# Kernel optimization log

Measured on AMD Instinct MI355X. Metric: run time of the kernel, lower is better.

Reference implementation:

```python
import jax, jax.numpy as jnp
import numpy as np

B, C, H, W, K = 32, 64, 112, 112, 5


def setup_inputs() -> dict:
    key = jax.random.key(0)
    kx, = jax.random.split(key, 1)
    x = jax.random.uniform(kx, (B, C, H, W), dtype=jnp.float32)
    # parameters per BioNorm.reset_parameters()
    sigma = jnp.ones((C,), jnp.float32)
    pow_p = jnp.full((C,), 2.0, jnp.float32)
    sum_kernel = jnp.full((C, 1, K, K), 1.0 / (K * K), jnp.float32)
    weight = jnp.ones((C,), jnp.float32)
    bias = jnp.zeros((C,), jnp.float32)
    return {"x": x, "sigma": sigma, "pow_p": pow_p, "sum_kernel": sum_kernel,
            "weight": weight, "bias": bias}


def _bionorm(x, sigma, pow_p, sum_kernel, weight, bias):
    s = sigma.reshape(1, -1, 1, 1)
    p = pow_p.reshape(1, -1, 1, 1)
    w = weight.reshape(1, -1, 1, 1)
    b = bias.reshape(1, -1, 1, 1)
    xp = x ** p  # [B,C,H,W]
    # depthwise (grouped) conv, VALID padding -> [B,C,H-K+1,W-K+1]
    sf = jax.lax.conv_general_dilated(
        xp, sum_kernel, window_strides=(1, 1), padding='VALID',
        feature_group_count=C,
        dimension_numbers=('NCHW', 'OIHW', 'NCHW'))
    hks = K // 2
    # replicate-pad back to [B,C,H,W]
    sf = jnp.pad(sf, ((0, 0), (0, 0), (hks, hks), (hks, hks)), mode='edge')
    den = s ** p + sf
    return w * xp / den + b


def reference(x, sigma, pow_p, sum_kernel, weight, bias):
    return _bionorm(x, sigma, pow_p, sum_kernel, weight, bias)
```

## Files before the change

### kernel.cpp

```cpp
#include <hip/hip_runtime.h>


#define Cch 64
#define Hh 112
#define Ww 112
#define TH 28
#define LROWS (TH + 4)
#define ST 116

__global__ __launch_bounds__(256) void bionorm_kernel(
    const float* __restrict__ x, const float* __restrict__ sigma,
    const float* __restrict__ pow_p, const float* __restrict__ sum_kernel,
    const float* __restrict__ weight, const float* __restrict__ bias,
    float* __restrict__ out)
{
    __shared__ float lds[LROWS * ST];

    const int rt  = blockIdx.x;
    const int c   = blockIdx.y;
    const int b   = blockIdx.z;
    const int tid = threadIdx.x;
    const int r0  = rt * TH;

    const float p  = pow_p[c];
    const float sg = sigma[c];
    const float wc = weight[c];
    const float bc = bias[c];
    const bool  p2 = (p == 2.0f);
    const float sp = p2 ? sg * sg : __powf(sg, p);

    float kw[25];
    const float* kp = sum_kernel + c * 25;
    #pragma unroll
    for (int j = 0; j < 25; ++j) kw[j] = kp[j];

    const float* xplane = x + ((size_t)(b * Cch + c)) * Hh * Ww;

    for (int i = tid; i < LROWS * 28; i += 256) {
        int s = i / 28, q = i - s * 28;
        int g = r0 - 2 + s;
        g = g < 0 ? 0 : (g > 111 ? 111 : g);
        const float4 v = *(const float4*)(xplane + g * Ww + q * 4);
        float4 xp;
        if (p2) {
            xp.x = v.x * v.x; xp.y = v.y * v.y;
            xp.z = v.z * v.z; xp.w = v.w * v.w;
        } else {
            xp.x = __powf(v.x, p); xp.y = __powf(v.y, p);
            xp.z = __powf(v.z, p); xp.w = __powf(v.w, p);
        }
        *(float4*)(&lds[s * ST + q * 4]) = xp;
    }
    __syncthreads();

    float* oplane = out + ((size_t)(b * Cch + c)) * Hh * Ww;

    for (int i = tid; i < TH * 28; i += 256) {
        int lr = i / 28, gq = i - lr * 28;
        int r  = r0 + lr;
        int w0 = gq * 4;

        int cr    = r  < 2 ? 2 : (r  > 109 ? 109 : r);
        int cwmin = w0 < 2 ? 2 : (w0 > 109 ? 109 : w0);
        int base  = cwmin - 2;
        int sRow  = cr - r0;

        float S0 = 0.f, S1 = 0.f, S2 = 0.f, S3 = 0.f;
        #pragma unroll
        for (int dy = 0; dy < 5; ++dy) {
            const float* row = &lds[(sRow + dy) * ST + base];
            float rv[8];
            #pragma unroll
            for (int t = 0; t < 8; ++t) rv[t] = row[t];
            #pragma unroll
            for (int dx = 0; dx < 5; ++dx) {
                float kv = kw[dy * 5 + dx];
                S0 = fmaf(kv, rv[dx + 0], S0);
                S1 = fmaf(kv, rv[dx + 1], S1);
                S2 = fmaf(kv, rv[dx + 2], S2);
                S3 = fmaf(kv, rv[dx + 3], S3);
            }
        }

        const float4 xp4 = *(const float4*)(&lds[(lr + 2) * ST + w0]);
        const float xv[4] = {xp4.x, xp4.y, xp4.z, xp4.w};

        float res[4];
        #pragma unroll
        for (int j = 0; j < 4; ++j) {
            int wj  = w0 + j;
            int cwj = wj < 2 ? 2 : (wj > 109 ? 109 : wj);
            int off = cwj - cwmin;
            float s_ = off == 0 ? S0 : off == 1 ? S1 : off == 2 ? S2 : S3;
            res[j] = fmaf(wc * xv[j], __builtin_amdgcn_rcpf(sp + s_), bc);
        }
        float4 o = {res[0], res[1], res[2], res[3]};
        *(float4*)(oplane + r * Ww + w0) = o;
    }
}

extern "C" void kernel_launch(void* const* d_in, const int* in_sizes, int n_in,
                              void* d_out, int out_size, void* d_ws, size_t ws_size,
                              hipStream_t stream) {
    const float* x          = (const float*)d_in[0];
    const float* sigma      = (const float*)d_in[1];
    const float* pow_p      = (const float*)d_in[2];
    const float* sum_kernel = (const float*)d_in[3];
    const float* weight     = (const float*)d_in[4];
    const float* bias       = (const float*)d_in[5];
    float* out = (float*)d_out;

    dim3 grid(4, Cch, 32);
    dim3 block(256);
    bionorm_kernel<<<grid, block, 0, stream>>>(x, sigma, pow_p, sum_kernel,
                                               weight, bias, out);
}
```

Before: 214.4 us.

## Register-block 28 outputs per thread with smaller 64-thread row tiles

```diff
diff --git a/kernel.cpp b/kernel.cpp
--- a/kernel.cpp
+++ b/kernel.cpp
@@ -4,11 +4,11 @@
 #define Cch 64
 #define Hh 112
 #define Ww 112
-#define TH 28
+#define TH 16
 #define LROWS (TH + 4)
-#define ST 116
+#define ST 114
 
-__global__ __launch_bounds__(256) void bionorm_kernel(
+__global__ __launch_bounds__(64) void bionorm_kernel(
     const float* __restrict__ x, const float* __restrict__ sigma,
     const float* __restrict__ pow_p, const float* __restrict__ sum_kernel,
     const float* __restrict__ weight, const float* __restrict__ bias,
@@ -36,11 +36,11 @@
 
     const float* xplane = x + ((size_t)(b * Cch + c)) * Hh * Ww;
 
-    for (int i = tid; i < LROWS * 28; i += 256) {
-        int s = i / 28, q = i - s * 28;
+    for (int i = tid; i < LROWS * 28; i += 64) {
+        int s = i / 28, q4 = i - s * 28;
         int g = r0 - 2 + s;
         g = g < 0 ? 0 : (g > 111 ? 111 : g);
-        const float4 v = *(const float4*)(xplane + g * Ww + q * 4);
+        const float4 v = *(const float4*)(xplane + g * Ww + q4 * 4);
         float4 xp;
         if (p2) {
             xp.x = v.x * v.x; xp.y = v.y * v.y;
@@ -49,53 +49,66 @@
             xp.x = __powf(v.x, p); xp.y = __powf(v.y, p);
             xp.z = __powf(v.z, p); xp.w = __powf(v.w, p);
         }
-        *(float4*)(&lds[s * ST + q * 4]) = xp;
+        *(float4*)(&lds[s * ST + q4 * 4]) = xp;
     }
     __syncthreads();
 
-    float* oplane = out + ((size_t)(b * Cch + c)) * Hh * Ww;
+    const int lr = tid >> 2;
+    const int q  = tid & 3;
+    const int r  = r0 + lr;
+    const int cr = r < 2 ? 2 : (r > 109 ? 109 : r);
+    const int crBase = cr - r0;
+    int base_t = 28 * q - 2;
+    base_t = base_t < 0 ? 0 : (base_t > 80 ? 80 : base_t);
 
-    for (int i = tid; i < TH * 28; i += 256) {
-        int lr = i / 28, gq = i - lr * 28;
-        int r  = r0 + lr;
-        int w0 = gq * 4;
+    float acc[28];
+    #pragma unroll
+    for (int j = 0; j < 28; ++j) acc[j] = 0.f;
 
-        int cr    = r  < 2 ? 2 : (r  > 109 ? 109 : r);
-        int cwmin = w0 < 2 ? 2 : (w0 > 109 ? 109 : w0);
-        int base  = cwmin - 2;
-        int sRow  = cr - r0;
+    #pragma unroll
+    for (int dy = 0; dy < 5; ++dy) {
+        const float* rowp = &lds[(crBase + dy) * ST + base_t];
+        float rv[32];
+        #pragma unroll
+        for (int t = 0; t < 16; ++t) {
+            const float2 v = *(const float2*)(rowp + 2 * t);
+            rv[2 * t] = v.x; rv[2 * t + 1] = v.y;
+        }
+        #pragma unroll
+        for (int dx = 0; dx < 5; ++dx) {
+            const float kv = kw[dy * 5 + dx];
+            #pragma unroll
+            for (int j = 0; j < 28; ++j)
+                acc[j] = fmaf(kv, rv[j + dx], acc[j]);
+        }
+    }
 
-        float S0 = 0.f, S1 = 0.f, S2 = 0.f, S3 = 0.f;
+    float sden[28];
+    if (q == 0) {
         #pragma unroll
-        for (int dy = 0; dy < 5; ++dy) {
-            const float* row = &lds[(sRow + dy) * ST + base];
-            float rv[8];
-            #pragma unroll
-            for (int t = 0; t < 8; ++t) rv[t] = row[t];
-            #pragma unroll
-            for (int dx = 0; dx < 5; ++dx) {
-                float kv = kw[dy * 5 + dx];
-                S0 = fmaf(kv, rv[dx + 0], S0);
-                S1 = fmaf(kv, rv[dx + 1], S1);
-                S2 = fmaf(kv, rv[dx + 2], S2);
-                S3 = fmaf(kv, rv[dx + 3], S3);
-            }
-        }
+        for (int i = 0; i < 28; ++i) sden[i] = acc[i < 2 ? 0 : i - 2];
+    } else if (q == 3) {
+        #pragma unroll
+        for (int i = 0; i < 28; ++i) sden[i] = acc[i > 25 ? 27 : i + 2];
+    } else {
+        #pragma unroll
+        for (int i = 0; i < 28; ++i) sden[i] = acc[i];
+    }
 
-        const float4 xp4 = *(const float4*)(&lds[(lr + 2) * ST + w0]);
-        const float xv[4] = {xp4.x, xp4.y, xp4.z, xp4.w};
+    const float* nump = &lds[(lr + 2) * ST + 28 * q];
+    float res[28];
+    #pragma unroll
+    for (int i = 0; i < 28; i += 2) {
+        const float2 nv = *(const float2*)(nump + i);
+        res[i]     = fmaf(wc * nv.x, __builtin_amdgcn_rcpf(sp + sden[i]),     bc);
+        res[i + 1] = fmaf(wc * nv.y, __builtin_amdgcn_rcpf(sp + sden[i + 1]), bc);
+    }
 
-        float res[4];
-        #pragma unroll
-        for (int j = 0; j < 4; ++j) {
-            int wj  = w0 + j;
-            int cwj = wj < 2 ? 2 : (wj > 109 ? 109 : wj);
-            int off = cwj - cwmin;
-            float s_ = off == 0 ? S0 : off == 1 ? S1 : off == 2 ? S2 : S3;
-            res[j] = fmaf(wc * xv[j], __builtin_amdgcn_rcpf(sp + s_), bc);
-        }
-        float4 o = {res[0], res[1], res[2], res[3]};
-        *(float4*)(oplane + r * Ww + w0) = o;
+    float* orow = out + ((size_t)(b * Cch + c)) * Hh * Ww + r * Ww + 28 * q;
+    #pragma unroll
+    for (int u = 0; u < 7; ++u) {
+        float4 o = {res[4 * u], res[4 * u + 1], res[4 * u + 2], res[4 * u + 3]};
+        *(float4*)(orow + 4 * u) = o;
     }
 }
 
@@ -110,8 +123,8 @@
     const float* bias       = (const float*)d_in[5];
     float* out = (float*)d_out;
 
-    dim3 grid(4, Cch, 32);
-    dim3 block(256);
+    dim3 grid(7, Cch, 32);
+    dim3 block(64);
     bionorm_kernel<<<grid, block, 0, stream>>>(x, sigma, pow_p, sum_kernel,
                                                weight, bias, out);
 }
```

Result: slower. 224.1 us (+4.5%).

## Use column-per-thread rolling 5x5 window with taller row tiles

Applied to the files above, without the earlier changes.

```diff
diff --git a/kernel.cpp b/kernel.cpp
--- a/kernel.cpp
+++ b/kernel.cpp
@@ -4,9 +4,75 @@
 #define Cch 64
 #define Hh 112
 #define Ww 112
-#define TH 28
+#define TH 56
 #define LROWS (TH + 4)
-#define ST 116
+#define STR 112
+
+template<int NITER, bool TOP, bool BOT>
+__device__ __forceinline__ void run_strip(
+    const float* lds, const float kw[25],
+    int r0, int rstart, int col, float sp, float wc, float bc,
+    float* __restrict__ oplane)
+{
+    const int cw   = col < 2 ? 2 : (col > 109 ? 109 : col);
+    const int base = cw - 2;
+    const int cidx = col - base;
+    const int cc0  = TOP ? 2 : rstart;
+    const bool store_ok = col < Ww;
+    const int lcol = col < Ww ? col : (Ww - 1);
+
+    float win[5][5];
+    #pragma unroll
+    for (int dy = 0; dy < 5; ++dy) {
+        const int s = cc0 - r0 + dy;
+        #pragma unroll
+        for (int dx = 0; dx < 5; ++dx)
+            win[dy][dx] = lds[s * STR + base + dx];
+    }
+
+    #pragma unroll
+    for (int i = 0; i < NITER; ++i) {
+        if (i > 0) {
+            const int s  = cc0 + i + 4 - r0;
+            const int ph = (i + 4) % 5;
+            #pragma unroll
+            for (int dx = 0; dx < 5; ++dx)
+                win[ph][dx] = lds[s * STR + base + dx];
+        }
+        float sum = 0.f;
+        #pragma unroll
+        for (int dy = 0; dy < 5; ++dy)
+            #pragma unroll
+            for (int dx = 0; dx < 5; ++dx)
+                sum = fmaf(kw[dy * 5 + dx], win[(i + dy) % 5][dx], sum);
+
+        const float* wrow = win[(i + 2) % 5];
+        float num = wrow[2];
+        if (cidx == 0) num = wrow[0];
+        else if (cidx == 1) num = wrow[1];
+        else if (cidx == 3) num = wrow[3];
+        else if (cidx == 4) num = wrow[4];
+
+        const int   cc   = cc0 + i;
+        const float invd = __builtin_amdgcn_rcpf(sp + sum);
+        if (store_ok) oplane[cc * Ww + col] = fmaf(wc * num, invd, bc);
+
+        if (TOP && i == 0) {
+            #pragma unroll
+            for (int r = 0; r < 2; ++r) {
+                const float n2 = lds[(r + 2) * STR + lcol];
+                if (store_ok) oplane[r * Ww + col] = fmaf(wc * n2, invd, bc);
+            }
+        }
+        if (BOT && i == NITER - 1) {
+            #pragma unroll
+            for (int r = 110; r < 112; ++r) {
+                const float n2 = lds[(r - r0 + 2) * STR + lcol];
+                if (store_ok) oplane[r * Ww + col] = fmaf(wc * n2, invd, bc);
+            }
+        }
+    }
+}
 
 __global__ __launch_bounds__(256) void bionorm_kernel(
     const float* __restrict__ x, const float* __restrict__ sigma,
@@ -14,7 +80,7 @@
     const float* __restrict__ weight, const float* __restrict__ bias,
     float* __restrict__ out)
 {
-    __shared__ float lds[LROWS * ST];
+    __shared__ float lds[LROWS * STR];
 
     const int rt  = blockIdx.x;
     const int c   = blockIdx.y;
@@ -49,54 +115,21 @@
             xp.x = __powf(v.x, p); xp.y = __powf(v.y, p);
             xp.z = __powf(v.z, p); xp.w = __powf(v.w, p);
         }
-        *(float4*)(&lds[s * ST + q * 4]) = xp;
+        *(float4*)(&lds[s * STR + q * 4]) = xp;
     }
     __syncthreads();
 
+    const int col    = tid & 127;
+    const int grp    = tid >> 7;
+    const int rstart = r0 + grp * 28;
     float* oplane = out + ((size_t)(b * Cch + c)) * Hh * Ww;
 
-    for (int i = tid; i < TH * 28; i += 256) {
-        int lr = i / 28, gq = i - lr * 28;
-        int r  = r0 + lr;
-        int w0 = gq * 4;
-
-        int cr    = r  < 2 ? 2 : (r  > 109 ? 109 : r);
-        int cwmin = w0 < 2 ? 2 : (w0 > 109 ? 109 : w0);
-        int base  = cwmin - 2;
-        int sRow  = cr - r0;
-
-        float S0 = 0.f, S1 = 0.f, S2 = 0.f, S3 = 0.f;
-        #pragma unroll
-        for (int dy = 0; dy < 5; ++dy) {
-            const float* row = &lds[(sRow + dy) * ST + base];
-            float rv[8];
-            #pragma unroll
-            for (int t = 0; t < 8; ++t) rv[t] = row[t];
-            #pragma unroll
-            for (int dx = 0; dx < 5; ++dx) {
-                float kv = kw[dy * 5 + dx];
-                S0 = fmaf(kv, rv[dx + 0], S0);
-                S1 = fmaf(kv, rv[dx + 1], S1);
-                S2 = fmaf(kv, rv[dx + 2], S2);
-                S3 = fmaf(kv, rv[dx + 3], S3);
-            }
-        }
-
-        const float4 xp4 = *(const float4*)(&lds[(lr + 2) * ST + w0]);
-        const float xv[4] = {xp4.x, xp4.y, xp4.z, xp4.w};
-
-        float res[4];
-        #pragma unroll
-        for (int j = 0; j < 4; ++j) {
-            int wj  = w0 + j;
-            int cwj = wj < 2 ? 2 : (wj > 109 ? 109 : wj);
-            int off = cwj - cwmin;
-            float s_ = off == 0 ? S0 : off == 1 ? S1 : off == 2 ? S2 : S3;
-            res[j] = fmaf(wc * xv[j], __builtin_amdgcn_rcpf(sp + s_), bc);
-        }
-        float4 o = {res[0], res[1], res[2], res[3]};
-        *(float4*)(oplane + r * Ww + w0) = o;
-    }
+    if (rstart == 0)
+        run_strip<26, true,  false>(lds, kw, r0, rstart, col, sp, wc, bc, oplane);
+    else if (rstart == 84)
+        run_strip<26, false, true >(lds, kw, r0, rstart, col, sp, wc, bc, oplane);
+    else
+        run_strip<28, false, false>(lds, kw, r0, rstart, col, sp, wc, bc, oplane);
 }
 
 extern "C" void kernel_launch(void* const* d_in, const int* in_sizes, int n_in,
@@ -110,7 +143,7 @@
     const float* bias       = (const float*)d_in[5];
     float* out = (float*)d_out;
 
-    dim3 grid(4, Cch, 32);
+    dim3 grid(2, Cch, 32);
     dim3 block(256);
     bionorm_kernel<<<grid, block, 0, stream>>>(x, sigma, pow_p, sum_kernel,
                                                weight, bias, out);
```

Result: slower. 287.9 us (+34.3%).
